# Performance work log

Hardware: AMD Instinct MI355X
Metric: run time of the kernel (lower is better)

## Reference

```python
import jax, jax.numpy as jnp
import numpy as np

H = 512   # embedding_dim (forced by Attention(512,512))
F = 21    # n_features
T = 28    # output_length

def _cell(x, h, c, Wih, Whh, b):
    # PyTorch LSTMCell math, gate order i,f,g,o
    g = x @ Wih.T + h @ Whh.T + b
    i, f, gg, o = jnp.split(g, 4, axis=-1)
    c2 = jax.nn.sigmoid(f) * c + jax.nn.sigmoid(i) * jnp.tanh(gg)
    h2 = jax.nn.sigmoid(o) * jnp.tanh(c2)
    return h2, c2

def _lstm3(inp, h, c, Wih0, Wih1, Wih2, Whh, bih, bhh):
    # 3-layer LSTM, single time step. h,c: [3,1,H]
    Wihs = (Wih0, Wih1, Wih2)
    hs, cs = [], []
    x = inp
    for l in range(3):
        hl, cl = _cell(x, h[l], c[l], Wihs[l], Whh[l], bih[l] + bhh[l])
        hs.append(hl); cs.append(cl)
        x = hl
    return x, jnp.stack(hs), jnp.stack(cs)

def setup_inputs() -> dict:
    key = jax.random.key(0)
    ks = jax.random.split(key, 20)
    s = 0.05
    f32 = jnp.float32
    return {
        "x": jax.random.normal(ks[0], (1, F), f32),
        "prev_y": jax.random.normal(ks[1], (1, F), f32),
        "enc_Wih0": jax.random.normal(ks[2], (4*H, F), f32) * s,
        "enc_Wih1": jax.random.normal(ks[3], (4*H, H), f32) * s,
        "enc_Wih2": jax.random.normal(ks[4], (4*H, H), f32) * s,
        "enc_Whh": jax.random.normal(ks[5], (3, 4*H, H), f32) * s,
        "enc_bih": jax.random.normal(ks[6], (3, 4*H), f32) * s,
        "enc_bhh": jax.random.normal(ks[7], (3, 4*H), f32) * s,
        "attn_W": jax.random.normal(ks[8], (H, 2*H), f32) * s,
        "attn_b": jax.random.normal(ks[9], (H,), f32) * s,
        "v_W": jax.random.normal(ks[10], (1, H), f32) * s,
        "dec_Wih0": jax.random.normal(ks[11], (4*H, H+F), f32) * s,
        "dec_Wih1": jax.random.normal(ks[12], (4*H, H), f32) * s,
        "dec_Wih2": jax.random.normal(ks[13], (4*H, H), f32) * s,
        "dec_Whh": jax.random.normal(ks[14], (3, 4*H, H), f32) * s,
        "dec_bih": jax.random.normal(ks[15], (3, 4*H), f32) * s,
        "dec_bhh": jax.random.normal(ks[16], (3, 4*H), f32) * s,
        "out_W": jax.random.normal(ks[17], (F, 2*H), f32) * s,
        "out_b": jax.random.normal(ks[18], (F,), f32) * s,
    }

def reference(x, prev_y, enc_Wih0, enc_Wih1, enc_Wih2, enc_Whh, enc_bih, enc_bhh,
              attn_W, attn_b, v_W, dec_Wih0, dec_Wih1, dec_Wih2, dec_Whh, dec_bih, dec_bhh,
              out_W, out_b):
    z = jnp.zeros((3, 1, H), x.dtype)
    # Encoder: single time step over feature-as-sequence input [1, F]
    enc_out, h, c = _lstm3(x, z, z, enc_Wih0, enc_Wih1, enc_Wih2, enc_Whh, enc_bih, enc_bhh)
    # enc_out: [1, H]; src_len == 1

    def step(carry, _):
        prev_out, h, c = carry
        # Bahdanau attention (src_len = 1)
        cat = jnp.concatenate([h[2], enc_out], axis=-1)          # [1, 2H]
        energy = jnp.tanh(cat @ attn_W.T + attn_b)               # [1, H]
        score = energy @ v_W.T                                    # [1, 1]
        a = jax.nn.softmax(score, axis=1)                         # [1, 1] (== 1)
        weighted = a * enc_out                                    # [1, H]
        rnn_in = jnp.concatenate([prev_out, weighted], axis=-1)  # [1, H+F]
        out, h2, c2 = _lstm3(rnn_in, h, c, dec_Wih0, dec_Wih1, dec_Wih2, dec_Whh, dec_bih, dec_bhh)
        y = jnp.concatenate([out, weighted], axis=-1) @ out_W.T + out_b  # [1, F]
        return (y, h2, c2), y

    _, ys = jax.lax.scan(step, (prev_y, h, c), None, length=T)
    return ys  # [T, 1, F]
```

## Files before the change

kernel.cpp:

```cpp
#include <hip/hip_runtime.h>
#include <cstddef>

constexpr int H  = 512;
constexpr int F  = 21;
constexpr int T  = 28;
constexpr int NB = 128;
constexpr int NT = 256;
constexpr int NW = NT / 64;

#define SCOPE_AGENT __HIP_MEMORY_SCOPE_AGENT

__device__ unsigned long long g_hp[2][3][H];
__device__ unsigned g_exit;

struct P {
  const float *x, *py, *eW0, *eW1, *eW2, *ebih, *ebhh;
  const float *dW0, *dW1, *dW2, *dWhh, *dbih, *dbhh, *outW, *outb;
  float* out;
};

__device__ __forceinline__ float sigm(float v)  { return 1.0f / (1.0f + __expf(-v)); }
__device__ __forceinline__ float tanh_f(float v){ return 1.0f - 2.0f / (__expf(2.0f * v) + 1.0f); }

__device__ __forceinline__ float4 wredsum4(float4 v) {
#pragma unroll
  for (int off = 32; off > 0; off >>= 1) {
    v.x += __shfl_xor(v.x, off, 64);
    v.y += __shfl_xor(v.y, off, 64);
    v.z += __shfl_xor(v.z, off, 64);
    v.w += __shfl_xor(v.w, off, 64);
  }
  return v;
}
__device__ __forceinline__ float wredsum1(float v) {
#pragma unroll
  for (int off = 32; off > 0; off >>= 1) v += __shfl_xor(v, off, 64);
  return v;
}

__device__ __forceinline__ void pput(unsigned long long* slot, float v, unsigned tag) {
  union { float f; unsigned u; } c; c.f = v;
  unsigned long long pk = ((unsigned long long)tag << 32) | (unsigned long long)c.u;
  (void)__hip_atomic_exchange(slot, pk, __ATOMIC_RELAXED, SCOPE_AGENT);
}
__device__ __forceinline__ unsigned long long tld(const unsigned long long* q) {
  return __hip_atomic_load(q, __ATOMIC_RELAXED, SCOPE_AGENT);
}
__device__ __forceinline__ float fbits(unsigned long long v) {
  union { unsigned u; float f; } c; c.u = (unsigned)v; return c.f;
}

__device__ __forceinline__ void stagev(const unsigned long long* __restrict__ A,
                                       unsigned wa, float* __restrict__ dst) {
  const int i = threadIdx.x;
  unsigned long long v0 = tld(A + i), v1 = tld(A + i + NT);
  int guard = 0;
  while ((((unsigned)(v0 >> 32)) != wa || ((unsigned)(v1 >> 32)) != wa) &&
         ++guard < (1 << 20)) {
    v0 = tld(A + i); v1 = tld(A + i + NT);
  }
  dst[i] = fbits(v0); dst[i + NT] = fbits(v1);
  __syncthreads();
}

__device__ __forceinline__ void pollvec8(const unsigned long long* __restrict__ A,
                                         int lane, unsigned want, float4& x0, float4& x1) {
  const unsigned long long* q = A + lane * 8;
  unsigned long long v[8];
#pragma unroll
  for (int k = 0; k < 8; ++k) v[k] = tld(q + k);
  int guard = 0;
  for (;;) {
    bool ok = true;
#pragma unroll
    for (int k = 0; k < 8; ++k) ok &= ((unsigned)(v[k] >> 32) == want);
    if (ok || ++guard > (1 << 20)) break;
#pragma unroll
    for (int k = 0; k < 8; ++k) v[k] = tld(q + k);
  }
  x0 = make_float4(fbits(v[0]), fbits(v[1]), fbits(v[2]), fbits(v[3]));
  x1 = make_float4(fbits(v[4]), fbits(v[5]), fbits(v[6]), fbits(v[7]));
}

struct W8 { float4 a[4]; float4 b[4]; };

__device__ __forceinline__ W8 ldw_g(const float* __restrict__ W, int r, int lane) {
  W8 o;
#pragma unroll
  for (int g = 0; g < 4; ++g) {
    const float* q = W + (size_t)(g * H + r) * H + lane * 8;
    o.a[g] = *(const float4*)q;
    o.b[g] = *(const float4*)(q + 4);
  }
  return o;
}
__device__ __forceinline__ W8 ldw_lds(const float* sM, int w, int lane) {
  W8 o;
#pragma unroll
  for (int g = 0; g < 4; ++g) {
    const float* q = sM + (w * 4 + g) * H + lane * 8;
    o.a[g] = *(const float4*)q;
    o.b[g] = *(const float4*)(q + 4);
  }
  return o;
}
__device__ __forceinline__ void fma8(const W8& wt, const float4& x0, const float4& x1,
                                     float s[4]) {
#pragma unroll
  for (int g = 0; g < 4; ++g) {
    s[g] += wt.a[g].x * x0.x + wt.a[g].y * x0.y + wt.a[g].z * x0.z + wt.a[g].w * x0.w
          + wt.b[g].x * x1.x + wt.b[g].y * x1.y + wt.b[g].z * x1.z + wt.b[g].w * x1.w;
  }
}

__device__ __forceinline__ float cellup(const float4& v, const float b[4], float& c) {
  float cn = sigm(v.y + b[1]) * c + sigm(v.x + b[0]) * tanh_f(v.z + b[2]);
  c = cn;
  return sigm(v.w + b[3]) * tanh_f(cn);
}

__device__ __forceinline__ void write_y(const P& p, int trow, int w, int lane,
                                        const float4& h0, const float4& h1,
                                        const float* sYe) {
  for (int j = w; j < F; j += NW) {
    const float* q = p.outW + (size_t)j * (2 * H) + lane * 8;
    float4 w0 = *(const float4*)q;
    float4 w1 = *(const float4*)(q + 4);
    float s = w0.x * h0.x + w0.y * h0.y + w0.z * h0.z + w0.w * h0.w
            + w1.x * h1.x + w1.y * h1.y + w1.z * h1.z + w1.w * h1.w;
    s = wredsum1(s);
    if (lane == 0) p.out[trow * F + j] = s + sYe[j];
  }
}

__global__ __launch_bounds__(NT, 1)
void k_flow(P p) {
  const int lane = threadIdx.x & 63;
  const int w    = threadIdx.x >> 6;
  const int r    = blockIdx.x * NW + w;

  __shared__ float sM[NW * 4 * H];
  __shared__ float sBuf[2][H];
  __shared__ float senc[H];
  __shared__ float sYe[F + 3];
  __shared__ int   s_last;

  float c0 = 0.f, c1 = 0.f, c2 = 0.f;
  float b00[4], b0p[4], b1s[4], b2s[4];
  float sOld0[4] = {0, 0, 0, 0}, sOld1[4] = {0, 0, 0, 0}, sOld2[4] = {0, 0, 0, 0};
  int bi = 0;

  {
    float s0 = 0.f, s1 = 0.f, s2 = 0.f, s3 = 0.f;
    if (lane < F) {
      const float xv = p.x[lane];
      s0 = p.eW0[(size_t)(0 * H + r) * F + lane] * xv;
      s1 = p.eW0[(size_t)(1 * H + r) * F + lane] * xv;
      s2 = p.eW0[(size_t)(2 * H + r) * F + lane] * xv;
      s3 = p.eW0[(size_t)(3 * H + r) * F + lane] * xv;
    }
    float4 v = wredsum4(make_float4(s0, s1, s2, s3));
    if (lane == 0) {
      const float* bi_ = p.ebih + r;
      const float* bh_ = p.ebhh + r;
      float cn = sigm(v.x + bi_[0] + bh_[0]) * tanh_f(v.z + bi_[2 * H] + bh_[2 * H]);
      c0 = cn;
      pput(&g_hp[1][0][r], sigm(v.w + bi_[3 * H] + bh_[3 * H]) * tanh_f(cn), 1u);
    }
  }

  {
    float4 mA[4], mB[4];
#pragma unroll
    for (int g = 0; g < 4; ++g) {
      mA[g] = make_float4(0.f, 0.f, 0.f, 0.f);
      mB[g] = make_float4(0.f, 0.f, 0.f, 0.f);
    }
    for (int f = 0; f < F; ++f) {
      const float* q = p.outW + (size_t)f * (2 * H) + lane * 8;
      const float4 oa = *(const float4*)q;
      const float4 ob = *(const float4*)(q + 4);
#pragma unroll
      for (int g = 0; g < 4; ++g) {
        const float wf = p.dW0[(size_t)(g * H + r) * (H + F) + f];
        mA[g].x += wf * oa.x; mA[g].y += wf * oa.y; mA[g].z += wf * oa.z; mA[g].w += wf * oa.w;
        mB[g].x += wf * ob.x; mB[g].y += wf * ob.y; mB[g].z += wf * ob.z; mB[g].w += wf * ob.w;
      }
    }
#pragma unroll
    for (int g = 0; g < 4; ++g) {
      *(float4*)(sM + (w * 4 + g) * H + lane * 8)     = mA[g];
      *(float4*)(sM + (w * 4 + g) * H + lane * 8 + 4) = mB[g];
    }
  }
#pragma unroll
  for (int g = 0; g < 4; ++g) {
    b1s[g] = p.dbih[4 * H + g * H + r] + p.dbhh[4 * H + g * H + r];
    b2s[g] = p.dbih[8 * H + g * H + r] + p.dbhh[8 * H + g * H + r];
  }

  {
    W8 wt = ldw_g(p.eW1, r, lane);
    stagev(g_hp[1][0], 1u, sBuf[0]);
    float4 a0 = *(const float4*)(sBuf[0] + lane * 8);
    float4 a1 = *(const float4*)(sBuf[0] + lane * 8 + 4);
    float s[4] = {0.f, 0.f, 0.f, 0.f};
    fma8(wt, a0, a1, s);
    float4 v = wredsum4(make_float4(s[0], s[1], s[2], s[3]));
    if (lane == 0) {
      const float* bi_ = p.ebih + 4 * H + r;
      const float* bh_ = p.ebhh + 4 * H + r;
      float cn = sigm(v.x + bi_[0] + bh_[0]) * tanh_f(v.z + bi_[2 * H] + bh_[2 * H]);
      c1 = cn;
      pput(&g_hp[1][1][r], sigm(v.w + bi_[3 * H] + bh_[3 * H]) * tanh_f(cn), 1u);
    }
  }

  {
    W8 wt  = ldw_g(p.eW2, r, lane);
    W8 wh1 = ldw_g(p.dWhh + (size_t)4 * H * H, r, lane);
    stagev(g_hp[1][1], 1u, sBuf[1]);
    float4 a0 = *(const float4*)(sBuf[1] + lane * 8);
    float4 a1 = *(const float4*)(sBuf[1] + lane * 8 + 4);
    float s[4] = {0.f, 0.f, 0.f, 0.f};
    fma8(wt, a0, a1, s);
    float4 v = wredsum4(make_float4(s[0], s[1], s[2], s[3]));
    if (lane == 0) {
      const float* bi_ = p.ebih + 8 * H + r;
      const float* bh_ = p.ebhh + 8 * H + r;
      float cn = sigm(v.x + bi_[0] + bh_[0]) * tanh_f(v.z + bi_[2 * H] + bh_[2 * H]);
      c2 = cn;
      pput(&g_hp[1][2][r], sigm(v.w + bi_[3 * H] + bh_[3 * H]) * tanh_f(cn), 1u);
    }
    fma8(wh1, a0, a1, sOld1);
  }

  {
    W8 wh2 = ldw_g(p.dWhh + (size_t)8 * H * H, r, lane);
    stagev(g_hp[1][2], 1u, senc);
    float4 e0 = *(const float4*)(senc + lane * 8);
    float4 e1 = *(const float4*)(senc + lane * 8 + 4);
    for (int j = w; j < F; j += NW) {
      const float* q = p.outW + (size_t)j * (2 * H) + H + lane * 8;
      float4 w0 = *(const float4*)q;
      float4 w1 = *(const float4*)(q + 4);
      float s = w0.x * e0.x + w0.y * e0.y + w0.z * e0.z + w0.w * e0.w
              + w1.x * e1.x + w1.y * e1.y + w1.z * e1.z + w1.w * e1.w;
      s = wredsum1(s);
      if (lane == 0) sYe[j] = s + p.outb[j];
    }
    {
      float sg[4];
#pragma unroll
      for (int g = 0; g < 4; ++g) {
        const float* q = p.dW0 + (size_t)(g * H + r) * (H + F) + F + lane * 8;
        sg[g] = q[0] * e0.x + q[1] * e0.y + q[2] * e0.z + q[3] * e0.w
              + q[4] * e1.x + q[5] * e1.y + q[6] * e1.z + q[7] * e1.w;
      }
      float4 v = wredsum4(make_float4(sg[0], sg[1], sg[2], sg[3]));
      if (lane == 0) {
        b0p[0] = v.x + p.dbih[0 * H + r] + p.dbhh[0 * H + r];
        b0p[1] = v.y + p.dbih[1 * H + r] + p.dbhh[1 * H + r];
        b0p[2] = v.z + p.dbih[2 * H + r] + p.dbhh[2 * H + r];
        b0p[3] = v.w + p.dbih[3 * H + r] + p.dbhh[3 * H + r];
      }
    }
    {
      float f0 = 0.f, f1 = 0.f, f2 = 0.f, f3 = 0.f;
      if (lane < F) {
        const float yv = p.py[lane];
        f0 = p.dW0[(size_t)(0 * H + r) * (H + F) + lane] * yv;
        f1 = p.dW0[(size_t)(1 * H + r) * (H + F) + lane] * yv;
        f2 = p.dW0[(size_t)(2 * H + r) * (H + F) + lane] * yv;
        f3 = p.dW0[(size_t)(3 * H + r) * (H + F) + lane] * yv;
      }
      float4 v = wredsum4(make_float4(f0, f1, f2, f3));
      if (lane == 0) {
        b00[0] = b0p[0] + v.x; b00[1] = b0p[1] + v.y;
        b00[2] = b0p[2] + v.z; b00[3] = b0p[3] + v.w;
      }
    }
    __syncthreads();
    {
      float f0 = 0.f, f1 = 0.f, f2 = 0.f, f3 = 0.f;
      if (lane < F) {
        const float yv = sYe[lane];
        f0 = p.dW0[(size_t)(0 * H + r) * (H + F) + lane] * yv;
        f1 = p.dW0[(size_t)(1 * H + r) * (H + F) + lane] * yv;
        f2 = p.dW0[(size_t)(2 * H + r) * (H + F) + lane] * yv;
        f3 = p.dW0[(size_t)(3 * H + r) * (H + F) + lane] * yv;
      }
      float4 v = wredsum4(make_float4(f0, f1, f2, f3));
      if (lane == 0) {
        b0p[0] += v.x; b0p[1] += v.y; b0p[2] += v.z; b0p[3] += v.w;
      }
    }
    fma8(wh2, e0, e1, sOld2);
  }

  {
    W8 wh0 = ldw_g(p.dWhh, r, lane);
    float4 a0 = *(const float4*)(sBuf[0] + lane * 8);
    float4 a1 = *(const float4*)(sBuf[0] + lane * 8 + 4);
    float s[4] = {0.f, 0.f, 0.f, 0.f};
    fma8(wh0, a0, a1, s);
    float4 v = wredsum4(make_float4(s[0], s[1], s[2], s[3]));
    if (lane == 0) pput(&g_hp[0][0][r], cellup(v, b00, c0), 2u);
  }
  __syncthreads();

  for (int t = 0; t < T; ++t) {
    const int pb = t & 1, ob = pb ^ 1;
    const unsigned wn = (unsigned)(t + 2);
    const unsigned wo = (unsigned)(t + 1);

    if (t >= 1) {
      W8 wh2 = ldw_g(p.dWhh + (size_t)8 * H * H, r, lane);
      stagev(g_hp[ob][2], wo, sBuf[bi]);
      W8 wm = ldw_lds(sM, w, lane);
      float4 h20 = *(const float4*)(sBuf[bi] + lane * 8);
      float4 h21 = *(const float4*)(sBuf[bi] + lane * 8 + 4);
      float s[4] = {sOld0[0], sOld0[1], sOld0[2], sOld0[3]};
      fma8(wm, h20, h21, s);
      float4 v = wredsum4(make_float4(s[0], s[1], s[2], s[3]));
      if (lane == 0) pput(&g_hp[pb][0][r], cellup(v, b0p, c0), wn);
      if (blockIdx.x == (unsigned)t) write_y(p, t - 1, w, lane, h20, h21, sYe);
      sOld2[0] = sOld2[1] = sOld2[2] = sOld2[3] = 0.f;
      fma8(wh2, h20, h21, sOld2);
      bi ^= 1;
    }

    {
      W8 wi  = ldw_g(p.dW1, r, lane);
      W8 wh0 = ldw_g(p.dWhh, r, lane);
      stagev(g_hp[pb][0], wn, sBuf[bi]);
      float4 a0 = *(const float4*)(sBuf[bi] + lane * 8);
      float4 a1 = *(const float4*)(sBuf[bi] + lane * 8 + 4);
      float s[4] = {sOld1[0], sOld1[1], sOld1[2], sOld1[3]};
      fma8(wi, a0, a1, s);
      float4 v = wredsum4(make_float4(s[0], s[1], s[2], s[3]));
      if (lane == 0) pput(&g_hp[pb][1][r], cellup(v, b1s, c1), wn);
      sOld0[0] = sOld0[1] = sOld0[2] = sOld0[3] = 0.f;
      fma8(wh0, a0, a1, sOld0);
      bi ^= 1;
    }
    {
      W8 wi  = ldw_g(p.dW2, r, lane);
      W8 wh1 = ldw_g(p.dWhh + (size_t)4 * H * H, r, lane);
      stagev(g_hp[pb][1], wn, sBuf[bi]);
      float4 a0 = *(const float4*)(sBuf[bi] + lane * 8);
      float4 a1 = *(const float4*)(sBuf[bi] + lane * 8 + 4);
      float s[4] = {sOld2[0], sOld2[1], sOld2[2], sOld2[3]};
      fma8(wi, a0, a1, s);
      float4 v = wredsum4(make_float4(s[0], s[1], s[2], s[3]));
      if (lane == 0) pput(&g_hp[pb][2][r], cellup(v, b2s, c2), wn);
      sOld1[0] = sOld1[1] = sOld1[2] = sOld1[3] = 0.f;
      fma8(wh1, a0, a1, sOld1);
      bi ^= 1;
    }
  }

  if (blockIdx.x == (unsigned)T) {
    float4 h20, h21;
    pollvec8(g_hp[(T - 1) & 1][2], lane, (unsigned)(T + 1), h20, h21);
    write_y(p, T - 1, w, lane, h20, h21, sYe);
  }

  __syncthreads();
  if (threadIdx.x == 0) {
    unsigned old = __hip_atomic_fetch_add(&g_exit, 1u, __ATOMIC_RELAXED, SCOPE_AGENT);
    s_last = (old == NB - 1) ? 1 : 0;
  }
  __syncthreads();
  if (s_last) {
    unsigned long long* z = &g_hp[0][0][0];
    for (int i = threadIdx.x; i < 2 * 3 * H; i += NT)
      __hip_atomic_store(z + i, 0ull, __ATOMIC_RELAXED, SCOPE_AGENT);
    if (threadIdx.x == 0)
      __hip_atomic_store(&g_exit, 0u, __ATOMIC_RELAXED, SCOPE_AGENT);
  }
}

extern "C" void kernel_launch(void* const* d_in, const int* in_sizes, int n_in,
                              void* d_out, int out_size, void* d_ws, size_t ws_size,
                              hipStream_t stream) {
  P p;
  p.x    = (const float*)d_in[0];
  p.py   = (const float*)d_in[1];
  p.eW0  = (const float*)d_in[2];
  p.eW1  = (const float*)d_in[3];
  p.eW2  = (const float*)d_in[4];
  p.ebih = (const float*)d_in[6];
  p.ebhh = (const float*)d_in[7];
  p.dW0  = (const float*)d_in[11];
  p.dW1  = (const float*)d_in[12];
  p.dW2  = (const float*)d_in[13];
  p.dWhh = (const float*)d_in[14];
  p.dbih = (const float*)d_in[15];
  p.dbhh = (const float*)d_in[16];
  p.outW = (const float*)d_in[17];
  p.outb = (const float*)d_in[18];
  p.out  = (float*)d_out;

  hipLaunchKernelGGL(k_flow, dim3(NB), dim3(NT), 0, stream, p);
}
```

Before: 356.5 us.

## Split persistent LSTM kernel into per-layer block groups with LDS-resident input weights

Blocks are now partitioned into three groups of 64, one per decoder layer, so each layer runs on its own set of blocks. This replaces the old scheme where every block handled one row of all three layers in sequence. Each warp owns two rows, and each block keeps its critical-path input weights in shared memory (the folded output-projection matrix for layer 0, the Wih slices for layers 1 and 2). The recurrent Whh product is computed off the critical path, after the layer's own hidden state is published. The aim is to pipeline the layers across time steps and shorten the per-step dependency chain. In exchange the block count rises to 192, adds cross-group flag polling, and relies on all blocks being co-resident.

```diff
diff --git a/kernel.cpp b/kernel.cpp
--- a/kernel.cpp
+++ b/kernel.cpp
@@ -4,7 +4,7 @@
 constexpr int H  = 512;
 constexpr int F  = 21;
 constexpr int T  = 28;
-constexpr int NB = 128;
+constexpr int NB = 192;
 constexpr int NT = 256;
 constexpr int NW = NT / 64;
 
@@ -83,7 +83,6 @@
 }
 
 struct W8 { float4 a[4]; float4 b[4]; };
-
 __device__ __forceinline__ W8 ldw_g(const float* __restrict__ W, int r, int lane) {
   W8 o;
 #pragma unroll
@@ -94,16 +93,6 @@
   }
   return o;
 }
-__device__ __forceinline__ W8 ldw_lds(const float* sM, int w, int lane) {
-  W8 o;
-#pragma unroll
-  for (int g = 0; g < 4; ++g) {
-    const float* q = sM + (w * 4 + g) * H + lane * 8;
-    o.a[g] = *(const float4*)q;
-    o.b[g] = *(const float4*)(q + 4);
-  }
-  return o;
-}
 __device__ __forceinline__ void fma8(const W8& wt, const float4& x0, const float4& x1,
                                      float s[4]) {
 #pragma unroll
@@ -111,6 +100,22 @@
     s[g] += wt.a[g].x * x0.x + wt.a[g].y * x0.y + wt.a[g].z * x0.z + wt.a[g].w * x0.w
           + wt.b[g].x * x1.x + wt.b[g].y * x1.y + wt.b[g].z * x1.z + wt.b[g].w * x1.w;
   }
+}
+
+__device__ __forceinline__ void dot2_lds(const float* __restrict__ wc, int i0, int lane,
+                                         const float* __restrict__ xb, float s[2][4]) {
+  float4 x0 = *(const float4*)(xb + lane * 8);
+  float4 x1 = *(const float4*)(xb + lane * 8 + 4);
+#pragma unroll
+  for (int j = 0; j < 2; ++j)
+#pragma unroll
+    for (int g = 0; g < 4; ++g) {
+      const float* q = wc + (size_t)((i0 + j) * 4 + g) * H + lane * 8;
+      float4 a = *(const float4*)q;
+      float4 b = *(const float4*)(q + 4);
+      s[j][g] += a.x * x0.x + a.y * x0.y + a.z * x0.z + a.w * x0.w
+               + b.x * x1.x + b.y * x1.y + b.z * x1.z + b.w * x1.w;
+    }
 }
 
 __device__ __forceinline__ float cellup(const float4& v, const float b[4], float& c) {
@@ -119,9 +124,9 @@
   return sigm(v.w + b[3]) * tanh_f(cn);
 }
 
-__device__ __forceinline__ void write_y(const P& p, int trow, int w, int lane,
-                                        const float4& h0, const float4& h1,
-                                        const float* sYe) {
+__device__ __forceinline__ void write_y_frag(const P& p, int trow, int w, int lane,
+                                             const float4& h0, const float4& h1,
+                                             const float* sYe) {
   for (int j = w; j < F; j += NW) {
     const float* q = p.outW + (size_t)j * (2 * H) + lane * 8;
     float4 w0 = *(const float4*)q;
@@ -137,109 +142,146 @@
 void k_flow(P p) {
   const int lane = threadIdx.x & 63;
   const int w    = threadIdx.x >> 6;
-  const int r    = blockIdx.x * NW + w;
-
-  __shared__ float sM[NW * 4 * H];
+  const int gid  = blockIdx.x >> 6;
+  const int bq   = blockIdx.x & 63;
+  const int i0   = w * 2;
+  const int rb   = bq * 8;
+  const int r0   = rb + i0;
+
+  __shared__ float wcrit[8 * 4 * H];
   __shared__ float sBuf[2][H];
+  __shared__ float sAux[H];
   __shared__ float senc[H];
   __shared__ float sYe[F + 3];
   __shared__ int   s_last;
 
-  float c0 = 0.f, c1 = 0.f, c2 = 0.f;
-  float b00[4], b0p[4], b1s[4], b2s[4];
-  float sOld0[4] = {0, 0, 0, 0}, sOld1[4] = {0, 0, 0, 0}, sOld2[4] = {0, 0, 0, 0};
-  int bi = 0;
-
-  {
-    float s0 = 0.f, s1 = 0.f, s2 = 0.f, s3 = 0.f;
-    if (lane < F) {
-      const float xv = p.x[lane];
-      s0 = p.eW0[(size_t)(0 * H + r) * F + lane] * xv;
-      s1 = p.eW0[(size_t)(1 * H + r) * F + lane] * xv;
-      s2 = p.eW0[(size_t)(2 * H + r) * F + lane] * xv;
-      s3 = p.eW0[(size_t)(3 * H + r) * F + lane] * xv;
-    }
-    float4 v = wredsum4(make_float4(s0, s1, s2, s3));
-    if (lane == 0) {
-      const float* bi_ = p.ebih + r;
-      const float* bh_ = p.ebhh + r;
-      float cn = sigm(v.x + bi_[0] + bh_[0]) * tanh_f(v.z + bi_[2 * H] + bh_[2 * H]);
-      c0 = cn;
-      pput(&g_hp[1][0][r], sigm(v.w + bi_[3 * H] + bh_[3 * H]) * tanh_f(cn), 1u);
-    }
-  }
-
-  {
-    float4 mA[4], mB[4];
-#pragma unroll
-    for (int g = 0; g < 4; ++g) {
-      mA[g] = make_float4(0.f, 0.f, 0.f, 0.f);
-      mB[g] = make_float4(0.f, 0.f, 0.f, 0.f);
-    }
-    for (int f = 0; f < F; ++f) {
-      const float* q = p.outW + (size_t)f * (2 * H) + lane * 8;
-      const float4 oa = *(const float4*)q;
-      const float4 ob = *(const float4*)(q + 4);
-#pragma unroll
-      for (int g = 0; g < 4; ++g) {
-        const float wf = p.dW0[(size_t)(g * H + r) * (H + F) + f];
-        mA[g].x += wf * oa.x; mA[g].y += wf * oa.y; mA[g].z += wf * oa.z; mA[g].w += wf * oa.w;
-        mB[g].x += wf * ob.x; mB[g].y += wf * ob.y; mB[g].z += wf * ob.z; mB[g].w += wf * ob.w;
-      }
-    }
-#pragma unroll
-    for (int g = 0; g < 4; ++g) {
-      *(float4*)(sM + (w * 4 + g) * H + lane * 8)     = mA[g];
-      *(float4*)(sM + (w * 4 + g) * H + lane * 8 + 4) = mB[g];
-    }
-  }
-#pragma unroll
-  for (int g = 0; g < 4; ++g) {
-    b1s[g] = p.dbih[4 * H + g * H + r] + p.dbhh[4 * H + g * H + r];
-    b2s[g] = p.dbih[8 * H + g * H + r] + p.dbhh[8 * H + g * H + r];
-  }
-
-  {
-    W8 wt = ldw_g(p.eW1, r, lane);
-    stagev(g_hp[1][0], 1u, sBuf[0]);
-    float4 a0 = *(const float4*)(sBuf[0] + lane * 8);
-    float4 a1 = *(const float4*)(sBuf[0] + lane * 8 + 4);
-    float s[4] = {0.f, 0.f, 0.f, 0.f};
-    fma8(wt, a0, a1, s);
-    float4 v = wredsum4(make_float4(s[0], s[1], s[2], s[3]));
-    if (lane == 0) {
-      const float* bi_ = p.ebih + 4 * H + r;
-      const float* bh_ = p.ebhh + 4 * H + r;
-      float cn = sigm(v.x + bi_[0] + bh_[0]) * tanh_f(v.z + bi_[2 * H] + bh_[2 * H]);
-      c1 = cn;
-      pput(&g_hp[1][1][r], sigm(v.w + bi_[3 * H] + bh_[3 * H]) * tanh_f(cn), 1u);
-    }
-  }
-
-  {
-    W8 wt  = ldw_g(p.eW2, r, lane);
-    W8 wh1 = ldw_g(p.dWhh + (size_t)4 * H * H, r, lane);
-    stagev(g_hp[1][1], 1u, sBuf[1]);
-    float4 a0 = *(const float4*)(sBuf[1] + lane * 8);
-    float4 a1 = *(const float4*)(sBuf[1] + lane * 8 + 4);
-    float s[4] = {0.f, 0.f, 0.f, 0.f};
-    fma8(wt, a0, a1, s);
-    float4 v = wredsum4(make_float4(s[0], s[1], s[2], s[3]));
-    if (lane == 0) {
-      const float* bi_ = p.ebih + 8 * H + r;
-      const float* bh_ = p.ebhh + 8 * H + r;
-      float cn = sigm(v.x + bi_[0] + bh_[0]) * tanh_f(v.z + bi_[2 * H] + bh_[2 * H]);
-      c2 = cn;
-      pput(&g_hp[1][2][r], sigm(v.w + bi_[3 * H] + bh_[3 * H]) * tanh_f(cn), 1u);
-    }
-    fma8(wh1, a0, a1, sOld1);
-  }
-
-  {
-    W8 wh2 = ldw_g(p.dWhh + (size_t)8 * H * H, r, lane);
+  float c[2] = {0.f, 0.f};
+  float sOld[2][4] = {{0, 0, 0, 0}, {0, 0, 0, 0}};
+  float bb[2][4];
+
+  if (gid == 0) {
+    {
+      float s[2][4] = {{0, 0, 0, 0}, {0, 0, 0, 0}};
+      if (lane < F) {
+        const float xv = p.x[lane];
+#pragma unroll
+        for (int j = 0; j < 2; ++j)
+#pragma unroll
+          for (int g = 0; g < 4; ++g)
+            s[j][g] = p.eW0[(size_t)(g * H + r0 + j) * F + lane] * xv;
+      }
+      float4 v0 = wredsum4(make_float4(s[0][0], s[0][1], s[0][2], s[0][3]));
+      float4 v1 = wredsum4(make_float4(s[1][0], s[1][1], s[1][2], s[1][3]));
+      if (lane == 0) {
+#pragma unroll
+        for (int j = 0; j < 2; ++j) {
+          const int r = r0 + j;
+          float be[4];
+#pragma unroll
+          for (int g = 0; g < 4; ++g) be[g] = p.ebih[g * H + r] + p.ebhh[g * H + r];
+          float4 v = j ? v1 : v0;
+          pput(&g_hp[1][0][r], cellup(v, be, c[j]), 1u);
+        }
+      }
+    }
+
+    {
+      float4 mA[2][4], mB[2][4];
+#pragma unroll
+      for (int j = 0; j < 2; ++j)
+#pragma unroll
+        for (int g = 0; g < 4; ++g) {
+          mA[j][g] = make_float4(0, 0, 0, 0);
+          mB[j][g] = make_float4(0, 0, 0, 0);
+        }
+      for (int f = 0; f < F; ++f) {
+        const float* q = p.outW + (size_t)f * (2 * H) + lane * 8;
+        const float4 oa = *(const float4*)q;
+        const float4 ob = *(const float4*)(q + 4);
+#pragma unroll
+        for (int j = 0; j < 2; ++j)
+#pragma unroll
+          for (int g = 0; g < 4; ++g) {
+            const float wf = p.dW0[(size_t)(g * H + r0 + j) * (H + F) + f];
+            mA[j][g].x += wf * oa.x; mA[j][g].y += wf * oa.y;
+            mA[j][g].z += wf * oa.z; mA[j][g].w += wf * oa.w;
+            mB[j][g].x += wf * ob.x; mB[j][g].y += wf * ob.y;
+            mB[j][g].z += wf * ob.z; mB[j][g].w += wf * ob.w;
+          }
+      }
+#pragma unroll
+      for (int j = 0; j < 2; ++j)
+#pragma unroll
+        for (int g = 0; g < 4; ++g) {
+          float* d = wcrit + (size_t)((i0 + j) * 4 + g) * H + lane * 8;
+          *(float4*)d = mA[j][g];
+          *(float4*)(d + 4) = mB[j][g];
+        }
+    }
+
+    {
+      W8 wh0 = ldw_g(p.dWhh, r0, lane);
+      W8 wh1 = ldw_g(p.dWhh, r0 + 1, lane);
+      stagev(g_hp[1][0], 1u, sAux);
+      float4 a0 = *(const float4*)(sAux + lane * 8);
+      float4 a1 = *(const float4*)(sAux + lane * 8 + 4);
+      fma8(wh0, a0, a1, sOld[0]);
+      fma8(wh1, a0, a1, sOld[1]);
+    }
+
     stagev(g_hp[1][2], 1u, senc);
     float4 e0 = *(const float4*)(senc + lane * 8);
     float4 e1 = *(const float4*)(senc + lane * 8 + 4);
+
+    float encb[2][4];
+    {
+      float sg[2][4];
+#pragma unroll
+      for (int j = 0; j < 2; ++j)
+#pragma unroll
+        for (int g = 0; g < 4; ++g) {
+          const float* q = p.dW0 + (size_t)(g * H + r0 + j) * (H + F) + F + lane * 8;
+          sg[j][g] = q[0] * e0.x + q[1] * e0.y + q[2] * e0.z + q[3] * e0.w
+                   + q[4] * e1.x + q[5] * e1.y + q[6] * e1.z + q[7] * e1.w;
+        }
+      float4 v0 = wredsum4(make_float4(sg[0][0], sg[0][1], sg[0][2], sg[0][3]));
+      float4 v1 = wredsum4(make_float4(sg[1][0], sg[1][1], sg[1][2], sg[1][3]));
+      const float vv0[4] = {v0.x, v0.y, v0.z, v0.w};
+      const float vv1[4] = {v1.x, v1.y, v1.z, v1.w};
+#pragma unroll
+      for (int g = 0; g < 4; ++g) {
+        encb[0][g] = vv0[g] + p.dbih[g * H + r0] + p.dbhh[g * H + r0];
+        encb[1][g] = vv1[g] + p.dbih[g * H + r0 + 1] + p.dbhh[g * H + r0 + 1];
+      }
+    }
+
+    {
+      float s[2][4] = {{0, 0, 0, 0}, {0, 0, 0, 0}};
+      if (lane < F) {
+        const float yv = p.py[lane];
+#pragma unroll
+        for (int j = 0; j < 2; ++j)
+#pragma unroll
+          for (int g = 0; g < 4; ++g)
+            s[j][g] = p.dW0[(size_t)(g * H + r0 + j) * (H + F) + lane] * yv;
+      }
+      float4 v0 = wredsum4(make_float4(s[0][0], s[0][1], s[0][2], s[0][3]));
+      float4 v1 = wredsum4(make_float4(s[1][0], s[1][1], s[1][2], s[1][3]));
+      if (lane == 0) {
+        const float pv0[4] = {v0.x, v0.y, v0.z, v0.w};
+        const float pv1[4] = {v1.x, v1.y, v1.z, v1.w};
+#pragma unroll
+        for (int j = 0; j < 2; ++j) {
+          float b00[4];
+#pragma unroll
+          for (int g = 0; g < 4; ++g)
+            b00[g] = encb[j][g] + (j ? pv1[g] : pv0[g]);
+          float4 v = make_float4(sOld[j][0], sOld[j][1], sOld[j][2], sOld[j][3]);
+          pput(&g_hp[0][0][r0 + j], cellup(v, b00, c[j]), 2u);
+        }
+      }
+    }
+
     for (int j = w; j < F; j += NW) {
       const float* q = p.outW + (size_t)j * (2 * H) + H + lane * 8;
       float4 w0 = *(const float4*)q;
@@ -249,121 +291,152 @@
       s = wredsum1(s);
       if (lane == 0) sYe[j] = s + p.outb[j];
     }
-    {
-      float sg[4];
-#pragma unroll
-      for (int g = 0; g < 4; ++g) {
-        const float* q = p.dW0 + (size_t)(g * H + r) * (H + F) + F + lane * 8;
-        sg[g] = q[0] * e0.x + q[1] * e0.y + q[2] * e0.z + q[3] * e0.w
-              + q[4] * e1.x + q[5] * e1.y + q[6] * e1.z + q[7] * e1.w;
-      }
-      float4 v = wredsum4(make_float4(sg[0], sg[1], sg[2], sg[3]));
-      if (lane == 0) {
-        b0p[0] = v.x + p.dbih[0 * H + r] + p.dbhh[0 * H + r];
-        b0p[1] = v.y + p.dbih[1 * H + r] + p.dbhh[1 * H + r];
-        b0p[2] = v.z + p.dbih[2 * H + r] + p.dbhh[2 * H + r];
-        b0p[3] = v.w + p.dbih[3 * H + r] + p.dbhh[3 * H + r];
-      }
-    }
-    {
-      float f0 = 0.f, f1 = 0.f, f2 = 0.f, f3 = 0.f;
-      if (lane < F) {
-        const float yv = p.py[lane];
-        f0 = p.dW0[(size_t)(0 * H + r) * (H + F) + lane] * yv;
-        f1 = p.dW0[(size_t)(1 * H + r) * (H + F) + lane] * yv;
-        f2 = p.dW0[(size_t)(2 * H + r) * (H + F) + lane] * yv;
-        f3 = p.dW0[(size_t)(3 * H + r) * (H + F) + lane] * yv;
-      }
-      float4 v = wredsum4(make_float4(f0, f1, f2, f3));
-      if (lane == 0) {
-        b00[0] = b0p[0] + v.x; b00[1] = b0p[1] + v.y;
-        b00[2] = b0p[2] + v.z; b00[3] = b0p[3] + v.w;
-      }
-    }
     __syncthreads();
     {
-      float f0 = 0.f, f1 = 0.f, f2 = 0.f, f3 = 0.f;
+      float s[2][4] = {{0, 0, 0, 0}, {0, 0, 0, 0}};
       if (lane < F) {
         const float yv = sYe[lane];
-        f0 = p.dW0[(size_t)(0 * H + r) * (H + F) + lane] * yv;
-        f1 = p.dW0[(size_t)(1 * H + r) * (H + F) + lane] * yv;
-        f2 = p.dW0[(size_t)(2 * H + r) * (H + F) + lane] * yv;
-        f3 = p.dW0[(size_t)(3 * H + r) * (H + F) + lane] * yv;
-      }
-      float4 v = wredsum4(make_float4(f0, f1, f2, f3));
+#pragma unroll
+        for (int j = 0; j < 2; ++j)
+#pragma unroll
+          for (int g = 0; g < 4; ++g)
+            s[j][g] = p.dW0[(size_t)(g * H + r0 + j) * (H + F) + lane] * yv;
+      }
+      float4 v0 = wredsum4(make_float4(s[0][0], s[0][1], s[0][2], s[0][3]));
+      float4 v1 = wredsum4(make_float4(s[1][0], s[1][1], s[1][2], s[1][3]));
+      const float pv0[4] = {v0.x, v0.y, v0.z, v0.w};
+      const float pv1[4] = {v1.x, v1.y, v1.z, v1.w};
+#pragma unroll
+      for (int g = 0; g < 4; ++g) {
+        bb[0][g] = encb[0][g] + pv0[g];
+        bb[1][g] = encb[1][g] + pv1[g];
+      }
+    }
+    {
+      W8 wh0 = ldw_g(p.dWhh, r0, lane);
+      W8 wh1 = ldw_g(p.dWhh, r0 + 1, lane);
+      __syncthreads();
+      stagev(g_hp[0][0], 2u, sAux);
+      float4 a0 = *(const float4*)(sAux + lane * 8);
+      float4 a1 = *(const float4*)(sAux + lane * 8 + 4);
+      sOld[0][0] = sOld[0][1] = sOld[0][2] = sOld[0][3] = 0.f;
+      sOld[1][0] = sOld[1][1] = sOld[1][2] = sOld[1][3] = 0.f;
+      fma8(wh0, a0, a1, sOld[0]);
+      fma8(wh1, a0, a1, sOld[1]);
+    }
+
+    for (int t = 1; t < T; ++t) {
+      float* xb = sBuf[t & 1];
+      stagev(g_hp[(t - 1) & 1][2], (unsigned)(t + 1), xb);
+      float s[2][4] = {{sOld[0][0], sOld[0][1], sOld[0][2], sOld[0][3]},
+                       {sOld[1][0], sOld[1][1], sOld[1][2], sOld[1][3]}};
+      dot2_lds(wcrit, i0, lane, xb, s);
+      float4 v0 = wredsum4(make_float4(s[0][0], s[0][1], s[0][2], s[0][3]));
+      float4 v1 = wredsum4(make_float4(s[1][0], s[1][1], s[1][2], s[1][3]));
       if (lane == 0) {
-        b0p[0] += v.x; b0p[1] += v.y; b0p[2] += v.z; b0p[3] += v.w;
-      }
-    }
-    fma8(wh2, e0, e1, sOld2);
-  }
-
-  {
-    W8 wh0 = ldw_g(p.dWhh, r, lane);
-    float4 a0 = *(const float4*)(sBuf[0] + lane * 8);
-    float4 a1 = *(const float4*)(sBuf[0] + lane * 8 + 4);
-    float s[4] = {0.f, 0.f, 0.f, 0.f};
-    fma8(wh0, a0, a1, s);
-    float4 v = wredsum4(make_float4(s[0], s[1], s[2], s[3]));
-    if (lane == 0) pput(&g_hp[0][0][r], cellup(v, b00, c0), 2u);
-  }
-  __syncthreads();
-
-  for (int t = 0; t < T; ++t) {
-    const int pb = t & 1, ob = pb ^ 1;
-    const unsigned wn = (unsigned)(t + 2);
-    const unsigned wo = (unsigned)(t + 1);
-
-    if (t >= 1) {
-      W8 wh2 = ldw_g(p.dWhh + (size_t)8 * H * H, r, lane);
-      stagev(g_hp[ob][2], wo, sBuf[bi]);
-      W8 wm = ldw_lds(sM, w, lane);
-      float4 h20 = *(const float4*)(sBuf[bi] + lane * 8);
-      float4 h21 = *(const float4*)(sBuf[bi] + lane * 8 + 4);
-      float s[4] = {sOld0[0], sOld0[1], sOld0[2], sOld0[3]};
-      fma8(wm, h20, h21, s);
-      float4 v = wredsum4(make_float4(s[0], s[1], s[2], s[3]));
-      if (lane == 0) pput(&g_hp[pb][0][r], cellup(v, b0p, c0), wn);
-      if (blockIdx.x == (unsigned)t) write_y(p, t - 1, w, lane, h20, h21, sYe);
-      sOld2[0] = sOld2[1] = sOld2[2] = sOld2[3] = 0.f;
-      fma8(wh2, h20, h21, sOld2);
-      bi ^= 1;
-    }
-
-    {
-      W8 wi  = ldw_g(p.dW1, r, lane);
-      W8 wh0 = ldw_g(p.dWhh, r, lane);
-      stagev(g_hp[pb][0], wn, sBuf[bi]);
-      float4 a0 = *(const float4*)(sBuf[bi] + lane * 8);
-      float4 a1 = *(const float4*)(sBuf[bi] + lane * 8 + 4);
-      float s[4] = {sOld1[0], sOld1[1], sOld1[2], sOld1[3]};
-      fma8(wi, a0, a1, s);
-      float4 v = wredsum4(make_float4(s[0], s[1], s[2], s[3]));
-      if (lane == 0) pput(&g_hp[pb][1][r], cellup(v, b1s, c1), wn);
-      sOld0[0] = sOld0[1] = sOld0[2] = sOld0[3] = 0.f;
-      fma8(wh0, a0, a1, sOld0);
-      bi ^= 1;
-    }
-    {
-      W8 wi  = ldw_g(p.dW2, r, lane);
-      W8 wh1 = ldw_g(p.dWhh + (size_t)4 * H * H, r, lane);
-      stagev(g_hp[pb][1], wn, sBuf[bi]);
-      float4 a0 = *(const float4*)(sBuf[bi] + lane * 8);
-      float4 a1 = *(const float4*)(sBuf[bi] + lane * 8 + 4);
-      float s[4] = {sOld2[0], sOld2[1], sOld2[2], sOld2[3]};
-      fma8(wi, a0, a1, s);
-      float4 v = wredsum4(make_float4(s[0], s[1], s[2], s[3]));
-      if (lane == 0) pput(&g_hp[pb][2][r], cellup(v, b2s, c2), wn);
-      sOld1[0] = sOld1[1] = sOld1[2] = sOld1[3] = 0.f;
-      fma8(wh1, a0, a1, sOld1);
-      bi ^= 1;
-    }
-  }
-
-  if (blockIdx.x == (unsigned)T) {
-    float4 h20, h21;
-    pollvec8(g_hp[(T - 1) & 1][2], lane, (unsigned)(T + 1), h20, h21);
-    write_y(p, T - 1, w, lane, h20, h21, sYe);
+        pput(&g_hp[t & 1][0][r0],     cellup(v0, bb[0], c[0]), (unsigned)(t + 2));
+        pput(&g_hp[t & 1][0][r0 + 1], cellup(v1, bb[1], c[1]), (unsigned)(t + 2));
+      }
+      if (bq == t) {
+        float4 h20 = *(const float4*)(xb + lane * 8);
+        float4 h21 = *(const float4*)(xb + lane * 8 + 4);
+        write_y_frag(p, t - 1, w, lane, h20, h21, sYe);
+      }
+      W8 wh0 = ldw_g(p.dWhh, r0, lane);
+      W8 wh1 = ldw_g(p.dWhh, r0 + 1, lane);
+      __syncthreads();
+      stagev(g_hp[t & 1][0], (unsigned)(t + 2), sAux);
+      float4 a0 = *(const float4*)(sAux + lane * 8);
+      float4 a1 = *(const float4*)(sAux + lane * 8 + 4);
+      sOld[0][0] = sOld[0][1] = sOld[0][2] = sOld[0][3] = 0.f;
+      sOld[1][0] = sOld[1][1] = sOld[1][2] = sOld[1][3] = 0.f;
+      fma8(wh0, a0, a1, sOld[0]);
+      fma8(wh1, a0, a1, sOld[1]);
+    }
+
+    if (bq == T) {
+      float4 h20, h21;
+      pollvec8(g_hp[(T - 1) & 1][2], lane, (unsigned)(T + 1), h20, h21);
+      write_y_frag(p, T - 1, w, lane, h20, h21, sYe);
+    }
+  } else {
+    const int l = gid;
+    const float* Wih  = (l == 1) ? p.dW1 : p.dW2;
+    const float* Whh  = p.dWhh + (size_t)l * 4 * H * H;
+    const float* eW   = (l == 1) ? p.eW1 : p.eW2;
+#pragma unroll
+    for (int j = 0; j < 2; ++j)
+#pragma unroll
+      for (int g = 0; g < 4; ++g)
+        bb[j][g] = p.dbih[l * 4 * H + g * H + r0 + j] + p.dbhh[l * 4 * H + g * H + r0 + j];
+
+    {
+      W8 we0 = ldw_g(eW, r0, lane);
+      W8 we1 = ldw_g(eW, r0 + 1, lane);
+      stagev(g_hp[1][l - 1], 1u, sBuf[0]);
+      float4 a0 = *(const float4*)(sBuf[0] + lane * 8);
+      float4 a1 = *(const float4*)(sBuf[0] + lane * 8 + 4);
+      float s[2][4] = {{0, 0, 0, 0}, {0, 0, 0, 0}};
+      fma8(we0, a0, a1, s[0]);
+      fma8(we1, a0, a1, s[1]);
+      float4 v0 = wredsum4(make_float4(s[0][0], s[0][1], s[0][2], s[0][3]));
+      float4 v1 = wredsum4(make_float4(s[1][0], s[1][1], s[1][2], s[1][3]));
+      if (lane == 0) {
+#pragma unroll
+        for (int j = 0; j < 2; ++j) {
+          const int r = r0 + j;
+          float be[4];
+#pragma unroll
+          for (int g = 0; g < 4; ++g)
+            be[g] = p.ebih[l * 4 * H + g * H + r] + p.ebhh[l * 4 * H + g * H + r];
+          float4 v = j ? v1 : v0;
+          pput(&g_hp[1][l][r], cellup(v, be, c[j]), 1u);
+        }
+      }
+    }
+
+    for (int u = threadIdx.x; u < 8 * 4 * (H / 4); u += NT) {
+      const int i   = u / (4 * (H / 4));
+      const int rem = u - i * 4 * (H / 4);
+      const int g   = rem / (H / 4);
+      const int k4  = rem - g * (H / 4);
+      const float4* src = (const float4*)(Wih + (size_t)(g * H + rb + i) * H) + k4;
+      ((float4*)(wcrit + (size_t)(i * 4 + g) * H))[k4] = *src;
+    }
+    {
+      W8 wh0 = ldw_g(Whh, r0, lane);
+      W8 wh1 = ldw_g(Whh, r0 + 1, lane);
+      stagev(g_hp[1][l], 1u, sAux);
+      float4 a0 = *(const float4*)(sAux + lane * 8);
+      float4 a1 = *(const float4*)(sAux + lane * 8 + 4);
+      fma8(wh0, a0, a1, sOld[0]);
+      fma8(wh1, a0, a1, sOld[1]);
+    }
+    __syncthreads();
+
+    for (int t = 0; t < T; ++t) {
+      float* xb = sBuf[t & 1];
+      stagev(g_hp[t & 1][l - 1], (unsigned)(t + 2), xb);
+      float s[2][4] = {{sOld[0][0], sOld[0][1], sOld[0][2], sOld[0][3]},
+                       {sOld[1][0], sOld[1][1], sOld[1][2], sOld[1][3]}};
+      dot2_lds(wcrit, i0, lane, xb, s);
+      float4 v0 = wredsum4(make_float4(s[0][0], s[0][1], s[0][2], s[0][3]));
+      float4 v1 = wredsum4(make_float4(s[1][0], s[1][1], s[1][2], s[1][3]));
+      if (lane == 0) {
+        pput(&g_hp[t & 1][l][r0],     cellup(v0, bb[0], c[0]), (unsigned)(t + 2));
+        pput(&g_hp[t & 1][l][r0 + 1], cellup(v1, bb[1], c[1]), (unsigned)(t + 2));
+      }
+      W8 wh0 = ldw_g(Whh, r0, lane);
+      W8 wh1 = ldw_g(Whh, r0 + 1, lane);
+      __syncthreads();
+      stagev(g_hp[t & 1][l], (unsigned)(t + 2), sAux);
+      float4 a0 = *(const float4*)(sAux + lane * 8);
+      float4 a1 = *(const float4*)(sAux + lane * 8 + 4);
+      sOld[0][0] = sOld[0][1] = sOld[0][2] = sOld[0][3] = 0.f;
+      sOld[1][0] = sOld[1][1] = sOld[1][2] = sOld[1][3] = 0.f;
+      fma8(wh0, a0, a1, sOld[0]);
+      fma8(wh1, a0, a1, sOld[1]);
+    }
   }
 
   __syncthreads();
```

Result: slower. 507.8 us (+42.4%).
